# Kernel optimization log

Measured on AMD Instinct MI355X. Metric: run time of the kernel, lower is better.

The kernel has to match this reference:

```python
import jax, jax.numpy as jnp
import numpy as np

HEADS = 8
DIM_HEAD = 32
SCALE = DIM_HEAD ** -0.5


def setup_inputs() -> dict:
    key = jax.random.key(0)
    k1, k2, k3 = jax.random.split(key, 3)
    B, L, H, W, C = 2, 5, 100, 176, 256
    inner = HEADS * DIM_HEAD  # 256
    x = jax.random.normal(k1, (B, L, H, W, C), dtype=jnp.float32)
    mask = jnp.ones((B, H, W, 1, L), dtype=jnp.float32)
    W_qkv = jax.random.normal(k2, (C, 3 * inner), dtype=jnp.float32) * (C ** -0.5)
    W_out = jax.random.normal(k3, (inner, C), dtype=jnp.float32) * (inner ** -0.5)
    b_out = jnp.zeros((C,), dtype=jnp.float32)
    return {"x": x, "mask": mask, "W_qkv": W_qkv, "W_out": W_out, "b_out": b_out}


def _cav_attention(x, mask, W_qkv, W_out, b_out):
    B, L, H, W, C = x.shape
    # (B, L, H, W, C) -> (B, H, W, L, C)
    xp = jnp.transpose(x, (0, 2, 3, 1, 4))
    qkv = xp @ W_qkv  # (B,H,W,L,3*inner)
    q, k, v = jnp.split(qkv, 3, axis=-1)

    def to_heads(t):  # (B,H,W,L,m*c) -> (B,m,H,W,L,c)
        t = t.reshape(B, H, W, L, HEADS, DIM_HEAD)
        return jnp.transpose(t, (0, 4, 1, 2, 3, 5))

    q, k, v = to_heads(q), to_heads(k), to_heads(v)
    att = jnp.einsum('bmhwic,bmhwjc->bmhwij', q, k) * SCALE
    # mask: (B,H,W,1,L) -> broadcast over heads as (B,1,H,W,1,L)
    att = jnp.where(mask[:, None] == 0, -jnp.inf, att)
    att = jax.nn.softmax(att, axis=-1)
    out = jnp.einsum('bmhwij,bmhwjc->bmhwic', att, v)
    # (B,m,H,W,L,c) -> (B,H,W,L,m*c)
    out = jnp.transpose(out, (0, 2, 3, 4, 1, 5)).reshape(B, H, W, L, HEADS * DIM_HEAD)
    out = out @ W_out + b_out  # dropout is identity in eval mode
    # (B,H,W,L,C) -> (B,L,H,W,C)
    return jnp.transpose(out, (0, 3, 1, 2, 4))


def reference(x, mask, W_qkv, W_out, b_out):
    return _cav_attention(x, mask, W_qkv, W_out, b_out)
```

## Files before the change

### kernel.cpp

```cpp
#include <hip/hip_runtime.h>
#include <hip/hip_bf16.h>

#define LQ 5
#define HQ 100
#define WQ 176
#define HWQ 17600
#define NT 35200
#define TPB 8
#define ROWS 40
#define NBLK 4400
#define SCALE_QK 0.17677669529663687f

#define AO_OFF 0
#define QBUF_OFF 20480
#define QBUF_STRIDE 7680
#define SMEM_BYTES 51200

typedef __attribute__((ext_vector_type(8))) short bf16x8;
typedef __attribute__((ext_vector_type(4))) float f32x4;
typedef __attribute__((ext_vector_type(2))) float f32x2;

__device__ __forceinline__ unsigned short f2bf(float f) {
  __hip_bfloat16 b = __float2bfloat16(f);
  return *(unsigned short*)&b;
}
__device__ __forceinline__ f32x2 bfpair(unsigned w) {
  union { unsigned u; float f; } lo, hi;
  lo.u = w << 16; hi.u = w & 0xffff0000u;
  return (f32x2){lo.f, hi.f};
}
__device__ __forceinline__ unsigned pack2(f32x2 v) {
  return ((unsigned)f2bf(v.y) << 16) | (unsigned)f2bf(v.x);
}
__device__ __forceinline__ int swzA(int row, int b) { return (row * 512 + b) ^ ((row & 7) << 4); }
__device__ __forceinline__ int swzQ(int row, int b) { return (row * 192 + b) ^ ((row & 7) << 4); }

__device__ __forceinline__ int row_gofs(int tile0, int r) {
  int gt = tile0 + r / 5;
  int l  = r - (r / 5) * 5;
  int b  = (gt >= HWQ) ? 1 : 0;
  int rem = gt - b * HWQ;
  return (((b * LQ + l) * HQ) * WQ + rem) << 8;
}

__global__ void prep_weights(const float* __restrict__ Wqkv,
                             const float* __restrict__ Wout,
                             unsigned short* __restrict__ WqkvT,
                             unsigned short* __restrict__ WoutT) {
  int idx = blockIdx.x * 256 + threadIdx.x;
  if (idx < 256 * 768) {
    int k = idx / 768, n = idx - k * 768;
    WqkvT[n * 256 + k] = f2bf(Wqkv[idx]);
  }
  if (idx < 256 * 256) {
    int k = idx >> 8, n = idx & 255;
    WoutT[n * 256 + k] = f2bf(Wout[idx]);
  }
}

__device__ __forceinline__ void do_head(int head, const char* AO, char* qb,
                                        const unsigned short* __restrict__ WqkvT,
                                        const float* __restrict__ mask, int tile0,
                                        int lr, int lg, int lane,
                                        unsigned* oPk ) {
  f32x4 acc[6][3];
  #pragma unroll
  for (int j = 0; j < 6; ++j)
    #pragma unroll
    for (int mt = 0; mt < 3; ++mt)
      acc[j][mt] = (f32x4){0.f, 0.f, 0.f, 0.f};

  const int hb = head * 32;
  const unsigned short* bp[6];
  bp[0] = WqkvT + (hb + lr) * 256 + lg * 8;
  bp[1] = WqkvT + (hb + 16 + lr) * 256 + lg * 8;
  bp[2] = WqkvT + (256 + hb + lr) * 256 + lg * 8;
  bp[3] = WqkvT + (256 + hb + 16 + lr) * 256 + lg * 8;
  bp[4] = WqkvT + (512 + hb + lr) * 256 + lg * 8;
  bp[5] = WqkvT + (512 + hb + 16 + lr) * 256 + lg * 8;

  bf16x8 bcur[6], bnxt[6];
  #pragma unroll
  for (int j = 0; j < 6; ++j) bcur[j] = *(const bf16x8*)(bp[j]);

  #pragma unroll
  for (int kt = 0; kt < 8; ++kt) {
    if (kt < 7) {
      #pragma unroll
      for (int j = 0; j < 6; ++j) bnxt[j] = *(const bf16x8*)(bp[j] + (kt + 1) * 32);
    }
    bf16x8 a0 = *(const bf16x8*)(AO + swzA(lr,      kt * 64 + lg * 16));
    bf16x8 a1 = *(const bf16x8*)(AO + swzA(16 + lr, kt * 64 + lg * 16));
    bf16x8 a2 = *(const bf16x8*)(AO + swzA(32 + lr, kt * 64 + lg * 16));
    #pragma unroll
    for (int j = 0; j < 6; ++j) {
      acc[j][0] = __builtin_amdgcn_mfma_f32_16x16x32_bf16(a0, bcur[j], acc[j][0], 0, 0, 0);
      acc[j][1] = __builtin_amdgcn_mfma_f32_16x16x32_bf16(a1, bcur[j], acc[j][1], 0, 0, 0);
      acc[j][2] = __builtin_amdgcn_mfma_f32_16x16x32_bf16(a2, bcur[j], acc[j][2], 0, 0, 0);
    }
    #pragma unroll
    for (int j = 0; j < 6; ++j) bcur[j] = bnxt[j];
  }

  #pragma unroll
  for (int j = 0; j < 6; ++j)
    #pragma unroll
    for (int mt = 0; mt < 3; ++mt)
      #pragma unroll
      for (int rg = 0; rg < 4; ++rg) {
        int row = mt * 16 + lg * 4 + rg;
        if (row < ROWS)
          *(unsigned short*)(qb + swzQ(row, (j * 16 + lr) * 2)) = f2bf(acc[j][mt][rg]);
      }

  if (lane < ROWS) {
    const int r = lane;
    const int t5 = (r / 5) * 5;
    const float* mrow = mask + (tile0 + r / 5) * 5;

    uint4 qa = *(const uint4*)(qb + swzQ(r, 0));
    uint4 qbv = *(const uint4*)(qb + swzQ(r, 16));
    uint4 qc = *(const uint4*)(qb + swzQ(r, 32));
    uint4 qd = *(const uint4*)(qb + swzQ(r, 48));
    f32x2 q2[16];
    q2[0]=bfpair(qa.x);  q2[1]=bfpair(qa.y);  q2[2]=bfpair(qa.z);  q2[3]=bfpair(qa.w);
    q2[4]=bfpair(qbv.x); q2[5]=bfpair(qbv.y); q2[6]=bfpair(qbv.z); q2[7]=bfpair(qbv.w);
    q2[8]=bfpair(qc.x);  q2[9]=bfpair(qc.y);  q2[10]=bfpair(qc.z); q2[11]=bfpair(qc.w);
    q2[12]=bfpair(qd.x); q2[13]=bfpair(qd.y); q2[14]=bfpair(qd.z); q2[15]=bfpair(qd.w);

    float p[5];
    #pragma unroll
    for (int j = 0; j < 5; ++j) {
      const int rk = t5 + j;
      uint4 ka = *(const uint4*)(qb + swzQ(rk, 64));
      uint4 kb = *(const uint4*)(qb + swzQ(rk, 80));
      uint4 kc = *(const uint4*)(qb + swzQ(rk, 96));
      uint4 kd = *(const uint4*)(qb + swzQ(rk, 112));
      f32x2 d2 = (f32x2){0.f, 0.f};
      d2 += q2[0]*bfpair(ka.x);  d2 += q2[1]*bfpair(ka.y);
      d2 += q2[2]*bfpair(ka.z);  d2 += q2[3]*bfpair(ka.w);
      d2 += q2[4]*bfpair(kb.x);  d2 += q2[5]*bfpair(kb.y);
      d2 += q2[6]*bfpair(kb.z);  d2 += q2[7]*bfpair(kb.w);
      d2 += q2[8]*bfpair(kc.x);  d2 += q2[9]*bfpair(kc.y);
      d2 += q2[10]*bfpair(kc.z); d2 += q2[11]*bfpair(kc.w);
      d2 += q2[12]*bfpair(kd.x); d2 += q2[13]*bfpair(kd.y);
      d2 += q2[14]*bfpair(kd.z); d2 += q2[15]*bfpair(kd.w);
      float d = (d2.x + d2.y) * SCALE_QK;
      p[j] = (mrow[j] == 0.0f) ? -1e30f : d;
    }
    float mx = fmaxf(fmaxf(fmaxf(p[0], p[1]), fmaxf(p[2], p[3])), p[4]);
    float sum = 0.f;
    #pragma unroll
    for (int j = 0; j < 5; ++j) { p[j] = __expf(p[j] - mx); sum += p[j]; }
    const float inv = 1.0f / sum;

    f32x2 o2[16];
    #pragma unroll
    for (int c = 0; c < 16; ++c) o2[c] = (f32x2){0.f, 0.f};
    #pragma unroll
    for (int j = 0; j < 5; ++j) {
      const int rv = t5 + j;
      uint4 va = *(const uint4*)(qb + swzQ(rv, 128));
      uint4 vb = *(const uint4*)(qb + swzQ(rv, 144));
      uint4 vc = *(const uint4*)(qb + swzQ(rv, 160));
      uint4 vd = *(const uint4*)(qb + swzQ(rv, 176));
      f32x2 pj2 = (f32x2){p[j], p[j]};
      o2[0]  += pj2*bfpair(va.x); o2[1]  += pj2*bfpair(va.y);
      o2[2]  += pj2*bfpair(va.z); o2[3]  += pj2*bfpair(va.w);
      o2[4]  += pj2*bfpair(vb.x); o2[5]  += pj2*bfpair(vb.y);
      o2[6]  += pj2*bfpair(vb.z); o2[7]  += pj2*bfpair(vb.w);
      o2[8]  += pj2*bfpair(vc.x); o2[9]  += pj2*bfpair(vc.y);
      o2[10] += pj2*bfpair(vc.z); o2[11] += pj2*bfpair(vc.w);
      o2[12] += pj2*bfpair(vd.x); o2[13] += pj2*bfpair(vd.y);
      o2[14] += pj2*bfpair(vd.z); o2[15] += pj2*bfpair(vd.w);
    }
    f32x2 inv2 = (f32x2){inv, inv};
    #pragma unroll
    for (int c = 0; c < 16; ++c) oPk[c] = pack2(o2[c] * inv2);
  }
}

__global__ __launch_bounds__(256, 2)
void cav_attn_fused(const float* __restrict__ x,
                    const float* __restrict__ mask,
                    const unsigned short* __restrict__ WqkvT,
                    const unsigned short* __restrict__ WoutT,
                    const float* __restrict__ b_out,
                    float* __restrict__ out) {
  extern __shared__ char smem[];
  char* AO = smem + AO_OFF;

  const int tid  = threadIdx.x;
  const int wave = tid >> 6;
  const int lane = tid & 63;
  const int lr   = lane & 15;
  const int lg   = lane >> 4;
  const int tile0 = blockIdx.x * TPB;

  #pragma unroll
  for (int i = 0; i < 10; ++i) {
    int r = i * 4 + wave;
    f32x4 v = *(const f32x4*)(x + row_gofs(tile0, r) + lane * 4);
    ushort4 pk;
    pk.x = f2bf(v[0]); pk.y = f2bf(v[1]); pk.z = f2bf(v[2]); pk.w = f2bf(v[3]);
    *(ushort4*)(AO + swzA(r, lane * 8)) = pk;
  }
  __syncthreads();

  char* qb = smem + QBUF_OFF + wave * QBUF_STRIDE;
  unsigned oPk0[16], oPk1[16];
  do_head(wave * 2,     AO, qb, WqkvT, mask, tile0, lr, lg, lane, oPk0);
  do_head(wave * 2 + 1, AO, qb, WqkvT, mask, tile0, lr, lg, lane, oPk1);

  __syncthreads();

  if (lane < ROWS) {
    const int r = lane;
    int b0 = (wave * 2) * 64;
    *(uint4*)(AO + swzA(r, b0))      = make_uint4(oPk0[0],  oPk0[1],  oPk0[2],  oPk0[3]);
    *(uint4*)(AO + swzA(r, b0 + 16)) = make_uint4(oPk0[4],  oPk0[5],  oPk0[6],  oPk0[7]);
    *(uint4*)(AO + swzA(r, b0 + 32)) = make_uint4(oPk0[8],  oPk0[9],  oPk0[10], oPk0[11]);
    *(uint4*)(AO + swzA(r, b0 + 48)) = make_uint4(oPk0[12], oPk0[13], oPk0[14], oPk0[15]);
    int b1 = (wave * 2 + 1) * 64;
    *(uint4*)(AO + swzA(r, b1))      = make_uint4(oPk1[0],  oPk1[1],  oPk1[2],  oPk1[3]);
    *(uint4*)(AO + swzA(r, b1 + 16)) = make_uint4(oPk1[4],  oPk1[5],  oPk1[6],  oPk1[7]);
    *(uint4*)(AO + swzA(r, b1 + 32)) = make_uint4(oPk1[8],  oPk1[9],  oPk1[10], oPk1[11]);
    *(uint4*)(AO + swzA(r, b1 + 48)) = make_uint4(oPk1[12], oPk1[13], oPk1[14], oPk1[15]);
  }
  __syncthreads();

  f32x4 acc2[4][3];
  #pragma unroll
  for (int j = 0; j < 4; ++j)
    #pragma unroll
    for (int mt = 0; mt < 3; ++mt)
      acc2[j][mt] = (f32x4){0.f, 0.f, 0.f, 0.f};

  const unsigned short* bp2[4];
  #pragma unroll
  for (int j = 0; j < 4; ++j)
    bp2[j] = WoutT + (wave * 64 + j * 16 + lr) * 256 + lg * 8;

  bf16x8 bcur2[4], bnxt2[4];
  #pragma unroll
  for (int j = 0; j < 4; ++j) bcur2[j] = *(const bf16x8*)(bp2[j]);

  #pragma unroll
  for (int kt = 0; kt < 8; ++kt) {
    if (kt < 7) {
      #pragma unroll
      for (int j = 0; j < 4; ++j) bnxt2[j] = *(const bf16x8*)(bp2[j] + (kt + 1) * 32);
    }
    bf16x8 a0 = *(const bf16x8*)(AO + swzA(lr,      kt * 64 + lg * 16));
    bf16x8 a1 = *(const bf16x8*)(AO + swzA(16 + lr, kt * 64 + lg * 16));
    bf16x8 a2 = *(const bf16x8*)(AO + swzA(32 + lr, kt * 64 + lg * 16));
    #pragma unroll
    for (int j = 0; j < 4; ++j) {
      acc2[j][0] = __builtin_amdgcn_mfma_f32_16x16x32_bf16(a0, bcur2[j], acc2[j][0], 0, 0, 0);
      acc2[j][1] = __builtin_amdgcn_mfma_f32_16x16x32_bf16(a1, bcur2[j], acc2[j][1], 0, 0, 0);
      acc2[j][2] = __builtin_amdgcn_mfma_f32_16x16x32_bf16(a2, bcur2[j], acc2[j][2], 0, 0, 0);
    }
    #pragma unroll
    for (int j = 0; j < 4; ++j) bcur2[j] = bnxt2[j];
  }
  __syncthreads();

  #pragma unroll
  for (int j = 0; j < 4; ++j) {
    const int col = wave * 64 + j * 16 + lr;
    const float bo = b_out[col];
    #pragma unroll
    for (int mt = 0; mt < 3; ++mt)
      #pragma unroll
      for (int rg = 0; rg < 4; ++rg) {
        int row = mt * 16 + lg * 4 + rg;
        if (row < ROWS)
          *(float*)(smem + row * 1024 + col * 4) = acc2[j][mt][rg] + bo;
      }
  }
  __syncthreads();
  #pragma unroll
  for (int i = 0; i < 10; ++i) {
    int r = i * 4 + wave;
    f32x4 v = *(const f32x4*)(smem + r * 1024 + lane * 16);
    *(f32x4*)(out + row_gofs(tile0, r) + lane * 4) = v;
  }
}

extern "C" void kernel_launch(void* const* d_in, const int* in_sizes, int n_in,
                              void* d_out, int out_size, void* d_ws, size_t ws_size,
                              hipStream_t stream) {
  (void)in_sizes; (void)n_in; (void)out_size; (void)ws_size;
  const float* x    = (const float*)d_in[0];
  const float* mask = (const float*)d_in[1];
  const float* Wqkv = (const float*)d_in[2];
  const float* Wout = (const float*)d_in[3];
  const float* bout = (const float*)d_in[4];
  float* out = (float*)d_out;

  unsigned short* WqkvT = (unsigned short*)d_ws;
  unsigned short* WoutT = WqkvT + 768 * 256;

  prep_weights<<<768, 256, 0, stream>>>(Wqkv, Wout, WqkvT, WoutT);
  cav_attn_fused<<<NBLK, 256, SMEM_BYTES, stream>>>(x, mask, WqkvT, WoutT, bout, out);
}
```

Measured before the change: 382.5 us.

## Stage per-head outputs in dedicated LDS buffer, use bf16 dot2, write output directly

Each head's attention output now goes into a separate swizzled LDS buffer, which removes one block-wide barrier and the register-held copy of the output. The QK dot product uses the bf16 fdot2 builtin, and the mask and row offsets are computed once per block into LDS. Weight prefetch now uses a two-deep register double buffer. The final projection is stored straight to global memory as scalar stores instead of being staged through LDS for coalesced vector writes. LDS per block grows from about 50KB to about 71KB, which may reduce occupancy, and the scalar stores may be less coalesced.

New measurement: 348.2 us. 9.0% less time.

```diff
diff --git a/kernel.cpp b/kernel.cpp
--- a/kernel.cpp
+++ b/kernel.cpp
@@ -14,7 +14,12 @@
 #define AO_OFF 0
 #define QBUF_OFF 20480
 #define QBUF_STRIDE 7680
-#define SMEM_BYTES 51200
+#define MASK_OFF 51200
+#define GOFS_OFF 51360
+#define OBUF_OFF 51520
+#define OBUF_WSTRIDE 5120
+#define OBUF_HSTRIDE 2560
+#define SMEM_BYTES 72512
 
 typedef __attribute__((ext_vector_type(8))) short bf16x8;
 typedef __attribute__((ext_vector_type(4))) float f32x4;
@@ -34,14 +39,21 @@
 }
 __device__ __forceinline__ int swzA(int row, int b) { return (row * 512 + b) ^ ((row & 7) << 4); }
 __device__ __forceinline__ int swzQ(int row, int b) { return (row * 192 + b) ^ ((row & 7) << 4); }
-
-__device__ __forceinline__ int row_gofs(int tile0, int r) {
-  int gt = tile0 + r / 5;
-  int l  = r - (r / 5) * 5;
-  int b  = (gt >= HWQ) ? 1 : 0;
-  int rem = gt - b * HWQ;
-  return (((b * LQ + l) * HQ) * WQ + rem) << 8;
-}
+__device__ __forceinline__ int swzO(int row, int b) { return row * 64 + (b ^ ((row & 3) << 4)); }
+
+#if __has_builtin(__builtin_amdgcn_fdot2_f32_bf16)
+typedef __attribute__((ext_vector_type(2))) __bf16 bf16x2v;
+__device__ __forceinline__ float dot2bf(unsigned a, unsigned b, float c) {
+  union { unsigned u; bf16x2v v; } ua, ub;
+  ua.u = a; ub.u = b;
+  return __builtin_amdgcn_fdot2_f32_bf16(ua.v, ub.v, c, false);
+}
+#else
+__device__ __forceinline__ float dot2bf(unsigned a, unsigned b, float c) {
+  f32x2 pa = bfpair(a), pb = bfpair(b);
+  return __builtin_fmaf(pa.y, pb.y, __builtin_fmaf(pa.x, pb.x, c));
+}
+#endif
 
 __global__ void prep_weights(const float* __restrict__ Wqkv,
                              const float* __restrict__ Wout,
@@ -58,11 +70,10 @@
   }
 }
 
-__device__ __forceinline__ void do_head(int head, const char* AO, char* qb,
+__device__ __forceinline__ void do_head(int head, const char* AO, char* qb, char* ob,
                                         const unsigned short* __restrict__ WqkvT,
-                                        const float* __restrict__ mask, int tile0,
-                                        int lr, int lg, int lane,
-                                        unsigned* oPk ) {
+                                        const float* maskb,
+                                        int lr, int lg, int lane) {
   f32x4 acc[6][3];
   #pragma unroll
   for (int j = 0; j < 6; ++j)
@@ -79,27 +90,32 @@
   bp[4] = WqkvT + (512 + hb + lr) * 256 + lg * 8;
   bp[5] = WqkvT + (512 + hb + 16 + lr) * 256 + lg * 8;
 
-  bf16x8 bcur[6], bnxt[6];
-  #pragma unroll
-  for (int j = 0; j < 6; ++j) bcur[j] = *(const bf16x8*)(bp[j]);
+  bf16x8 bb0[6], bb1[6];
+  #pragma unroll
+  for (int j = 0; j < 6; ++j) {
+    bb0[j] = *(const bf16x8*)(bp[j]);
+    bb1[j] = *(const bf16x8*)(bp[j] + 32);
+  }
 
   #pragma unroll
   for (int kt = 0; kt < 8; ++kt) {
-    if (kt < 7) {
-      #pragma unroll
-      for (int j = 0; j < 6; ++j) bnxt[j] = *(const bf16x8*)(bp[j] + (kt + 1) * 32);
-    }
     bf16x8 a0 = *(const bf16x8*)(AO + swzA(lr,      kt * 64 + lg * 16));
     bf16x8 a1 = *(const bf16x8*)(AO + swzA(16 + lr, kt * 64 + lg * 16));
     bf16x8 a2 = *(const bf16x8*)(AO + swzA(32 + lr, kt * 64 + lg * 16));
     #pragma unroll
     for (int j = 0; j < 6; ++j) {
-      acc[j][0] = __builtin_amdgcn_mfma_f32_16x16x32_bf16(a0, bcur[j], acc[j][0], 0, 0, 0);
-      acc[j][1] = __builtin_amdgcn_mfma_f32_16x16x32_bf16(a1, bcur[j], acc[j][1], 0, 0, 0);
-      acc[j][2] = __builtin_amdgcn_mfma_f32_16x16x32_bf16(a2, bcur[j], acc[j][2], 0, 0, 0);
-    }
-    #pragma unroll
-    for (int j = 0; j < 6; ++j) bcur[j] = bnxt[j];
+      bf16x8 bv = (kt & 1) ? bb1[j] : bb0[j];
+      acc[j][0] = __builtin_amdgcn_mfma_f32_16x16x32_bf16(a0, bv, acc[j][0], 0, 0, 0);
+      acc[j][1] = __builtin_amdgcn_mfma_f32_16x16x32_bf16(a1, bv, acc[j][1], 0, 0, 0);
+      acc[j][2] = __builtin_amdgcn_mfma_f32_16x16x32_bf16(a2, bv, acc[j][2], 0, 0, 0);
+    }
+    if (kt < 6) {
+      #pragma unroll
+      for (int j = 0; j < 6; ++j) {
+        bf16x8 nl = *(const bf16x8*)(bp[j] + (kt + 2) * 32);
+        if (kt & 1) bb1[j] = nl; else bb0[j] = nl;
+      }
+    }
   }
 
   #pragma unroll
@@ -116,43 +132,37 @@
   if (lane < ROWS) {
     const int r = lane;
     const int t5 = (r / 5) * 5;
-    const float* mrow = mask + (tile0 + r / 5) * 5;
-
-    uint4 qa = *(const uint4*)(qb + swzQ(r, 0));
-    uint4 qbv = *(const uint4*)(qb + swzQ(r, 16));
-    uint4 qc = *(const uint4*)(qb + swzQ(r, 32));
-    uint4 qd = *(const uint4*)(qb + swzQ(r, 48));
-    f32x2 q2[16];
-    q2[0]=bfpair(qa.x);  q2[1]=bfpair(qa.y);  q2[2]=bfpair(qa.z);  q2[3]=bfpair(qa.w);
-    q2[4]=bfpair(qbv.x); q2[5]=bfpair(qbv.y); q2[6]=bfpair(qbv.z); q2[7]=bfpair(qbv.w);
-    q2[8]=bfpair(qc.x);  q2[9]=bfpair(qc.y);  q2[10]=bfpair(qc.z); q2[11]=bfpair(qc.w);
-    q2[12]=bfpair(qd.x); q2[13]=bfpair(qd.y); q2[14]=bfpair(qd.z); q2[15]=bfpair(qd.w);
+    uint4 q0 = *(const uint4*)(qb + swzQ(r, 0));
+    uint4 q1 = *(const uint4*)(qb + swzQ(r, 16));
+    uint4 q2 = *(const uint4*)(qb + swzQ(r, 32));
+    uint4 q3 = *(const uint4*)(qb + swzQ(r, 48));
 
     float p[5];
     #pragma unroll
     for (int j = 0; j < 5; ++j) {
       const int rk = t5 + j;
-      uint4 ka = *(const uint4*)(qb + swzQ(rk, 64));
-      uint4 kb = *(const uint4*)(qb + swzQ(rk, 80));
-      uint4 kc = *(const uint4*)(qb + swzQ(rk, 96));
-      uint4 kd = *(const uint4*)(qb + swzQ(rk, 112));
-      f32x2 d2 = (f32x2){0.f, 0.f};
-      d2 += q2[0]*bfpair(ka.x);  d2 += q2[1]*bfpair(ka.y);
-      d2 += q2[2]*bfpair(ka.z);  d2 += q2[3]*bfpair(ka.w);
-      d2 += q2[4]*bfpair(kb.x);  d2 += q2[5]*bfpair(kb.y);
-      d2 += q2[6]*bfpair(kb.z);  d2 += q2[7]*bfpair(kb.w);
-      d2 += q2[8]*bfpair(kc.x);  d2 += q2[9]*bfpair(kc.y);
-      d2 += q2[10]*bfpair(kc.z); d2 += q2[11]*bfpair(kc.w);
-      d2 += q2[12]*bfpair(kd.x); d2 += q2[13]*bfpair(kd.y);
-      d2 += q2[14]*bfpair(kd.z); d2 += q2[15]*bfpair(kd.w);
-      float d = (d2.x + d2.y) * SCALE_QK;
-      p[j] = (mrow[j] == 0.0f) ? -1e30f : d;
+      uint4 k0 = *(const uint4*)(qb + swzQ(rk, 64));
+      uint4 k1 = *(const uint4*)(qb + swzQ(rk, 80));
+      uint4 k2 = *(const uint4*)(qb + swzQ(rk, 96));
+      uint4 k3 = *(const uint4*)(qb + swzQ(rk, 112));
+      float d = 0.f;
+      d = dot2bf(q0.x, k0.x, d); d = dot2bf(q0.y, k0.y, d);
+      d = dot2bf(q0.z, k0.z, d); d = dot2bf(q0.w, k0.w, d);
+      d = dot2bf(q1.x, k1.x, d); d = dot2bf(q1.y, k1.y, d);
+      d = dot2bf(q1.z, k1.z, d); d = dot2bf(q1.w, k1.w, d);
+      d = dot2bf(q2.x, k2.x, d); d = dot2bf(q2.y, k2.y, d);
+      d = dot2bf(q2.z, k2.z, d); d = dot2bf(q2.w, k2.w, d);
+      d = dot2bf(q3.x, k3.x, d); d = dot2bf(q3.y, k3.y, d);
+      d = dot2bf(q3.z, k3.z, d); d = dot2bf(q3.w, k3.w, d);
+      p[j] = d * SCALE_QK + maskb[rk];
     }
     float mx = fmaxf(fmaxf(fmaxf(p[0], p[1]), fmaxf(p[2], p[3])), p[4]);
     float sum = 0.f;
     #pragma unroll
     for (int j = 0; j < 5; ++j) { p[j] = __expf(p[j] - mx); sum += p[j]; }
     const float inv = 1.0f / sum;
+    #pragma unroll
+    for (int j = 0; j < 5; ++j) p[j] *= inv;
 
     f32x2 o2[16];
     #pragma unroll
@@ -160,23 +170,28 @@
     #pragma unroll
     for (int j = 0; j < 5; ++j) {
       const int rv = t5 + j;
-      uint4 va = *(const uint4*)(qb + swzQ(rv, 128));
-      uint4 vb = *(const uint4*)(qb + swzQ(rv, 144));
-      uint4 vc = *(const uint4*)(qb + swzQ(rv, 160));
-      uint4 vd = *(const uint4*)(qb + swzQ(rv, 176));
+      uint4 v0 = *(const uint4*)(qb + swzQ(rv, 128));
+      uint4 v1 = *(const uint4*)(qb + swzQ(rv, 144));
+      uint4 v2 = *(const uint4*)(qb + swzQ(rv, 160));
+      uint4 v3 = *(const uint4*)(qb + swzQ(rv, 176));
       f32x2 pj2 = (f32x2){p[j], p[j]};
-      o2[0]  += pj2*bfpair(va.x); o2[1]  += pj2*bfpair(va.y);
-      o2[2]  += pj2*bfpair(va.z); o2[3]  += pj2*bfpair(va.w);
-      o2[4]  += pj2*bfpair(vb.x); o2[5]  += pj2*bfpair(vb.y);
-      o2[6]  += pj2*bfpair(vb.z); o2[7]  += pj2*bfpair(vb.w);
-      o2[8]  += pj2*bfpair(vc.x); o2[9]  += pj2*bfpair(vc.y);
-      o2[10] += pj2*bfpair(vc.z); o2[11] += pj2*bfpair(vc.w);
-      o2[12] += pj2*bfpair(vd.x); o2[13] += pj2*bfpair(vd.y);
-      o2[14] += pj2*bfpair(vd.z); o2[15] += pj2*bfpair(vd.w);
-    }
-    f32x2 inv2 = (f32x2){inv, inv};
-    #pragma unroll
-    for (int c = 0; c < 16; ++c) oPk[c] = pack2(o2[c] * inv2);
+      o2[0]  += pj2 * bfpair(v0.x); o2[1]  += pj2 * bfpair(v0.y);
+      o2[2]  += pj2 * bfpair(v0.z); o2[3]  += pj2 * bfpair(v0.w);
+      o2[4]  += pj2 * bfpair(v1.x); o2[5]  += pj2 * bfpair(v1.y);
+      o2[6]  += pj2 * bfpair(v1.z); o2[7]  += pj2 * bfpair(v1.w);
+      o2[8]  += pj2 * bfpair(v2.x); o2[9]  += pj2 * bfpair(v2.y);
+      o2[10] += pj2 * bfpair(v2.z); o2[11] += pj2 * bfpair(v2.w);
+      o2[12] += pj2 * bfpair(v3.x); o2[13] += pj2 * bfpair(v3.y);
+      o2[14] += pj2 * bfpair(v3.z); o2[15] += pj2 * bfpair(v3.w);
+    }
+    unsigned oPk[16];
+    #pragma unroll
+    for (int c = 0; c < 16; ++c) oPk[c] = pack2(o2[c]);
+    const int sx = (r & 3) << 4;
+    *(uint4*)(ob + r * 64 + (0 ^ sx))  = make_uint4(oPk[0],  oPk[1],  oPk[2],  oPk[3]);
+    *(uint4*)(ob + r * 64 + (16 ^ sx)) = make_uint4(oPk[4],  oPk[5],  oPk[6],  oPk[7]);
+    *(uint4*)(ob + r * 64 + (32 ^ sx)) = make_uint4(oPk[8],  oPk[9],  oPk[10], oPk[11]);
+    *(uint4*)(ob + r * 64 + (48 ^ sx)) = make_uint4(oPk[12], oPk[13], oPk[14], oPk[15]);
   }
 }
 
@@ -188,7 +203,9 @@
                     const float* __restrict__ b_out,
                     float* __restrict__ out) {
   extern __shared__ char smem[];
-  char* AO = smem + AO_OFF;
+  char*  AO    = smem + AO_OFF;
+  float* maskb = (float*)(smem + MASK_OFF);
+  int*   gofs  = (int*)(smem + GOFS_OFF);
 
   const int tid  = threadIdx.x;
   const int wave = tid >> 6;
@@ -197,10 +214,21 @@
   const int lg   = lane >> 4;
   const int tile0 = blockIdx.x * TPB;
 
+  if (lane < ROWS) {
+    int tt = lane / LQ;
+    int l  = lane - tt * LQ;
+    int gt = tile0 + tt;
+    int b  = (gt >= HWQ) ? 1 : 0;
+    int rem = gt - b * HWQ;
+    gofs[lane] = (((b * LQ + l) * HQ) * WQ + rem) << 8;
+    float mv = mask[gt * LQ + l];
+    maskb[lane] = (mv == 0.0f) ? -1e30f : 0.0f;
+  }
+
   #pragma unroll
   for (int i = 0; i < 10; ++i) {
     int r = i * 4 + wave;
-    f32x4 v = *(const f32x4*)(x + row_gofs(tile0, r) + lane * 4);
+    f32x4 v = *(const f32x4*)(x + gofs[r] + lane * 4);
     ushort4 pk;
     pk.x = f2bf(v[0]); pk.y = f2bf(v[1]); pk.z = f2bf(v[2]); pk.w = f2bf(v[3]);
     *(ushort4*)(AO + swzA(r, lane * 8)) = pk;
@@ -208,25 +236,9 @@
   __syncthreads();
 
   char* qb = smem + QBUF_OFF + wave * QBUF_STRIDE;
-  unsigned oPk0[16], oPk1[16];
-  do_head(wave * 2,     AO, qb, WqkvT, mask, tile0, lr, lg, lane, oPk0);
-  do_head(wave * 2 + 1, AO, qb, WqkvT, mask, tile0, lr, lg, lane, oPk1);
-
-  __syncthreads();
-
-  if (lane < ROWS) {
-    const int r = lane;
-    int b0 = (wave * 2) * 64;
-    *(uint4*)(AO + swzA(r, b0))      = make_uint4(oPk0[0],  oPk0[1],  oPk0[2],  oPk0[3]);
-    *(uint4*)(AO + swzA(r, b0 + 16)) = make_uint4(oPk0[4],  oPk0[5],  oPk0[6],  oPk0[7]);
-    *(uint4*)(AO + swzA(r, b0 + 32)) = make_uint4(oPk0[8],  oPk0[9],  oPk0[10], oPk0[11]);
-    *(uint4*)(AO + swzA(r, b0 + 48)) = make_uint4(oPk0[12], oPk0[13], oPk0[14], oPk0[15]);
-    int b1 = (wave * 2 + 1) * 64;
-    *(uint4*)(AO + swzA(r, b1))      = make_uint4(oPk1[0],  oPk1[1],  oPk1[2],  oPk1[3]);
-    *(uint4*)(AO + swzA(r, b1 + 16)) = make_uint4(oPk1[4],  oPk1[5],  oPk1[6],  oPk1[7]);
-    *(uint4*)(AO + swzA(r, b1 + 32)) = make_uint4(oPk1[8],  oPk1[9],  oPk1[10], oPk1[11]);
-    *(uint4*)(AO + swzA(r, b1 + 48)) = make_uint4(oPk1[12], oPk1[13], oPk1[14], oPk1[15]);
-  }
+  char* ob = smem + OBUF_OFF + wave * OBUF_WSTRIDE;
+  do_head(wave * 2,     AO, qb, ob,                WqkvT, maskb, lr, lg, lane);
+  do_head(wave * 2 + 1, AO, qb, ob + OBUF_HSTRIDE, WqkvT, maskb, lr, lg, lane);
   __syncthreads();
 
   f32x4 acc2[4][3];
@@ -241,29 +253,34 @@
   for (int j = 0; j < 4; ++j)
     bp2[j] = WoutT + (wave * 64 + j * 16 + lr) * 256 + lg * 8;
 
-  bf16x8 bcur2[4], bnxt2[4];
-  #pragma unroll
-  for (int j = 0; j < 4; ++j) bcur2[j] = *(const bf16x8*)(bp2[j]);
+  bf16x8 cc0[4], cc1[4];
+  #pragma unroll
+  for (int j = 0; j < 4; ++j) {
+    cc0[j] = *(const bf16x8*)(bp2[j]);
+    cc1[j] = *(const bf16x8*)(bp2[j] + 32);
+  }
 
   #pragma unroll
   for (int kt = 0; kt < 8; ++kt) {
-    if (kt < 7) {
+    const char* OB = smem + OBUF_OFF + (kt >> 1) * OBUF_WSTRIDE + (kt & 1) * OBUF_HSTRIDE;
+    bf16x8 a0 = *(const bf16x8*)(OB + swzO(lr,      lg * 16));
+    bf16x8 a1 = *(const bf16x8*)(OB + swzO(16 + lr, lg * 16));
+    bf16x8 a2 = *(const bf16x8*)(OB + swzO(32 + lr, lg * 16));
+    #pragma unroll
+    for (int j = 0; j < 4; ++j) {
+      bf16x8 bv = (kt & 1) ? cc1[j] : cc0[j];
+      acc2[j][0] = __builtin_amdgcn_mfma_f32_16x16x32_bf16(a0, bv, acc2[j][0], 0, 0, 0);
+      acc2[j][1] = __builtin_amdgcn_mfma_f32_16x16x32_bf16(a1, bv, acc2[j][1], 0, 0, 0);
+      acc2[j][2] = __builtin_amdgcn_mfma_f32_16x16x32_bf16(a2, bv, acc2[j][2], 0, 0, 0);
+    }
+    if (kt < 6) {
       #pragma unroll
-      for (int j = 0; j < 4; ++j) bnxt2[j] = *(const bf16x8*)(bp2[j] + (kt + 1) * 32);
-    }
-    bf16x8 a0 = *(const bf16x8*)(AO + swzA(lr,      kt * 64 + lg * 16));
-    bf16x8 a1 = *(const bf16x8*)(AO + swzA(16 + lr, kt * 64 + lg * 16));
-    bf16x8 a2 = *(const bf16x8*)(AO + swzA(32 + lr, kt * 64 + lg * 16));
-    #pragma unroll
-    for (int j = 0; j < 4; ++j) {
-      acc2[j][0] = __builtin_amdgcn_mfma_f32_16x16x32_bf16(a0, bcur2[j], acc2[j][0], 0, 0, 0);
-      acc2[j][1] = __builtin_amdgcn_mfma_f32_16x16x32_bf16(a1, bcur2[j], acc2[j][1], 0, 0, 0);
-      acc2[j][2] = __builtin_amdgcn_mfma_f32_16x16x32_bf16(a2, bcur2[j], acc2[j][2], 0, 0, 0);
-    }
-    #pragma unroll
-    for (int j = 0; j < 4; ++j) bcur2[j] = bnxt2[j];
-  }
-  __syncthreads();
+      for (int j = 0; j < 4; ++j) {
+        bf16x8 nl = *(const bf16x8*)(bp2[j] + (kt + 2) * 32);
+        if (kt & 1) cc1[j] = nl; else cc0[j] = nl;
+      }
+    }
+  }
 
   #pragma unroll
   for (int j = 0; j < 4; ++j) {
@@ -275,15 +292,8 @@
       for (int rg = 0; rg < 4; ++rg) {
         int row = mt * 16 + lg * 4 + rg;
         if (row < ROWS)
-          *(float*)(smem + row * 1024 + col * 4) = acc2[j][mt][rg] + bo;
+          out[gofs[row] + col] = acc2[j][mt][rg] + bo;
       }
-  }
-  __syncthreads();
-  #pragma unroll
-  for (int i = 0; i < 10; ++i) {
-    int r = i * 4 + wave;
-    f32x4 v = *(const f32x4*)(smem + r * 1024 + lane * 16);
-    *(f32x4*)(out + row_gofs(tile0, r) + lane * 4) = v;
   }
 }
 
@@ -301,6 +311,9 @@
   unsigned short* WqkvT = (unsigned short*)d_ws;
   unsigned short* WoutT = WqkvT + 768 * 256;
 
+  (void)hipFuncSetAttribute((const void*)cav_attn_fused,
+                            hipFuncAttributeMaxDynamicSharedMemorySize, SMEM_BYTES);
+
   prep_weights<<<768, 256, 0, stream>>>(Wqkv, Wout, WqkvT, WoutT);
   cav_attn_fused<<<NBLK, 256, SMEM_BYTES, stream>>>(x, mask, WqkvT, WoutT, bout, out);
 }
```
